# Kernel tuning notes

Measured on AMD Instinct MI355X. Metric: run time of the kernel, lower is better.

## Reference

```python
import jax, jax.numpy as jnp
import numpy as np

B, S, E = 2, 2048, 2048
H, KV, HD = 16, 4, 128  # num_heads, num_kv_heads, head_dim
G = H // KV             # query heads per kv head
ROPE_BASE = 10000.0


def rope_tables(dim, maxlen):
    freqs = 1.0 / ROPE_BASE ** (jnp.arange(0, dim, 2, dtype=jnp.float32) / dim)
    t = jnp.arange(maxlen, dtype=jnp.float32)
    f = jnp.outer(t, freqs)  # (maxlen, dim//2)
    return jnp.cos(f), jnp.sin(f)


def apply_rope(x, cos, sin):
    # x: (..., seq, heads, head_dim); interleaved-pair rotation
    s_len = x.shape[-3]
    c = cos[:s_len][:, None, :]
    s = sin[:s_len][:, None, :]
    x1 = x[..., ::2]
    x2 = x[..., 1::2]
    return jnp.stack([x1 * c - x2 * s, x1 * s + x2 * c], axis=-1).reshape(x.shape)


def setup_inputs() -> dict:
    key = jax.random.key(0)
    kx, kq, kk, kv, ko = jax.random.split(key, 5)
    x = jax.random.normal(kx, (B, S, E), dtype=jnp.float32)
    Wq = jax.random.normal(kq, (E, H * HD), dtype=jnp.float32) * 0.02
    Wk = jax.random.normal(kk, (E, KV * HD), dtype=jnp.float32) * 0.02
    Wv = jax.random.normal(kv, (E, KV * HD), dtype=jnp.float32) * 0.02
    Wo = jax.random.normal(ko, (H * HD, E), dtype=jnp.float32) * 0.02
    mask = jnp.tril(jnp.ones((S, S), dtype=bool))[None, None]  # causal (1,1,S,S)
    return {"x": x, "Wq": Wq, "Wk": Wk, "Wv": Wv, "Wo": Wo, "mask": mask}


def reference(x, Wq, Wk, Wv, Wo, mask):
    b, s, _ = x.shape
    cos, sin = rope_tables(HD, s)
    q = (x @ Wq).reshape(b, s, H, HD)
    k = (x @ Wk).reshape(b, s, KV, HD)
    v = (x @ Wv).reshape(b, s, KV, HD)
    q = apply_rope(q, cos, sin)
    k = apply_rope(k, cos, sin)
    if G > 1:
        k = jnp.repeat(k, G, axis=2)  # (b, s, H, HD)
        v = jnp.repeat(v, G, axis=2)
    q = jnp.transpose(q, (0, 2, 1, 3))  # (b, H, s, HD)
    k = jnp.transpose(k, (0, 2, 1, 3))
    v = jnp.transpose(v, (0, 2, 1, 3))
    scale = jnp.sqrt(jnp.float32(HD)).astype(q.dtype)
    scores = jnp.einsum("bhqd,bhkd->bhqk", q, k) / scale
    scores = jnp.where(mask, scores, jnp.finfo(scores.dtype).min)
    attn = jax.nn.softmax(scores, axis=-1)
    out = jnp.einsum("bhqk,bhkd->bhqd", attn, v)
    out = jnp.transpose(out, (0, 2, 1, 3)).reshape(b, s, H * HD)
    return out @ Wo
```

## Files before the change

kernel.cpp:

```cpp
#include <hip/hip_runtime.h>
#include <hip/hip_bf16.h>
#include <cstdint>

#define B_ 2
#define S_ 2048
#define E_ 2048
#define H_ 16
#define KV_ 4
#define HD_ 128
#define BS_ (B_*S_)
#define QKV_LD 3072
#define SM_SCALE 0.08838834764831845f
#define SC_LOG2E 0.1275424488538497f

typedef __attribute__((ext_vector_type(8))) __bf16 bf16x8;
typedef __attribute__((ext_vector_type(4))) float  floatx4;

__device__ __forceinline__ unsigned short f2bf(float f) {
  union { float f; unsigned u; } v; v.f = f;
  unsigned r = v.u + 0x7fffu + ((v.u >> 16) & 1u);
  return (unsigned short)(r >> 16);
}
__device__ __forceinline__ float bf2f(unsigned short u) {
  union { unsigned u; float f; } v; v.u = ((unsigned)u) << 16; return v.f;
}

__device__ __forceinline__ void async_cp16(const void* g, void* l) {
  __builtin_amdgcn_global_load_lds(
      (const __attribute__((address_space(1))) void*)g,
      (__attribute__((address_space(3))) void*)l, 16, 0, 0);
}

__global__ __launch_bounds__(256)
void cvt_bf16(const float* __restrict__ src, unsigned short* __restrict__ dst,
              int n4) {
  int idx = blockIdx.x * 256 + threadIdx.x;
  if (idx >= n4) return;
  float4 v = *(const float4*)(src + (size_t)idx * 4);
  ushort4 o;
  o.x = f2bf(v.x); o.y = f2bf(v.y); o.z = f2bf(v.z); o.w = f2bf(v.w);
  *(ushort4*)(dst + (size_t)idx * 4) = o;
}

__global__ __launch_bounds__(256)
void cvt_bf16_t(const float* __restrict__ src, unsigned short* __restrict__ dst,
                int N, int dld, int noff) {
  __shared__ float tile[64 * 65];
  const int t = threadIdx.x;
  const int bk = blockIdx.y * 64, bn = blockIdx.x * 64;
  const int r = t >> 2, cg = t & 3;
#pragma unroll
  for (int i = 0; i < 4; ++i) {
    int c = cg * 16 + i * 4;
    float4 v = *(const float4*)(src + (size_t)(bk + r) * N + bn + c);
    tile[r * 65 + c] = v.x; tile[r * 65 + c + 1] = v.y;
    tile[r * 65 + c + 2] = v.z; tile[r * 65 + c + 3] = v.w;
  }
  __syncthreads();
  const int nl = t >> 2, kg = t & 3;
  union { unsigned short u[16]; uint4 q[2]; } o;
#pragma unroll
  for (int j = 0; j < 16; ++j)
    o.u[j] = f2bf(tile[(kg * 16 + j) * 65 + nl]);
  unsigned short* dp = dst + (size_t)(noff + bn + nl) * dld + bk + kg * 16;
  *(uint4*)(dp) = o.q[0];
  *(uint4*)(dp + 8) = o.q[1];
}

__global__ __launch_bounds__(256)
void rope_kernel(unsigned short* __restrict__ qkv) {
  const int PPR = 1280;
  int idx = blockIdx.x * 256 + threadIdx.x;
  if (idx >= BS_ * PPR) return;
  int row = idx / PPR, p = idx - row * PPR;
  int col = (p < 1024) ? (2 * p) : (2048 + 2 * (p - 1024));
  int d = p & 63;
  int s = row & (S_ - 1);
  float freq = expf(-(float)d * 0.14391156831212787f);
  float ang = (float)s * freq;
  float c = cosf(ang), sn = sinf(ang);
  unsigned short* ptr = qkv + (size_t)row * QKV_LD + col;
  float x1 = bf2f(ptr[0]), x2 = bf2f(ptr[1]);
  ptr[0] = f2bf(x1 * c - x2 * sn);
  ptr[1] = f2bf(x1 * sn + x2 * c);
}

__global__ __launch_bounds__(256)
void vtrans_kernel(const unsigned short* __restrict__ qkv,
                   unsigned short* __restrict__ vt) {
  __shared__ unsigned short tile[64 * 72];
  const int tid = threadIdx.x;
  const int s0 = blockIdx.x * 64;
  const int g = blockIdx.y >> 1;
  const int hh = (blockIdx.y & 1) * 64;
  const int b = g >> 2, kvh = g & 3;
#pragma unroll
  for (int i = 0; i < 2; ++i) {
    int chunk = tid + i * 256;
    int r = chunk >> 3, c = (chunk & 7) * 8;
    uint4 v = *(const uint4*)(qkv + (size_t)(b * S_ + s0 + r) * QKV_LD + 2560 + kvh * HD_ + hh + c);
    *(uint4*)(tile + r * 72 + c) = v;
  }
  __syncthreads();
#pragma unroll
  for (int i = 0; i < 2; ++i) {
    int chunk = tid + i * 256;
    int hdr = chunk >> 3, sc = (chunk & 7) * 8;
    union { unsigned short u[8]; uint4 v; } t;
#pragma unroll
    for (int j = 0; j < 8; ++j) t.u[j] = tile[(sc + j) * 72 + hdr];
    *(uint4*)(vt + (size_t)(g * HD_ + hh + hdr) * S_ + s0 + sc) = t.v;
  }
}

template<bool OUT_BF16>
__global__ __launch_bounds__(256, 2)
void gemm_tn(const unsigned short* __restrict__ A,
             const unsigned short* __restrict__ BT,
             void* __restrict__ C, int M, int N, int K) {
  __shared__ unsigned short Ash[128 * 32];
  __shared__ unsigned short Bsh[128 * 32];
  const int tid = threadIdx.x;
  const int l = tid & 63;
  const int l16 = l & 15, l4 = l >> 4;
  const int wave = tid >> 6;
  const int wm = (wave >> 1) * 64, wn = (wave & 1) * 64;
  const int bm = blockIdx.y * 128, bn = blockIdx.x * 128;

  const int srow = l >> 2;
  const int sg = (((l & 3) - (l >> 4)) & 3) * 8;

  floatx4 acc[4][4] = {};

  for (int kb = 0; kb < K; kb += 32) {
    __syncthreads();
#pragma unroll
    for (int i = 0; i < 2; ++i) {
      int cc = wave + i * 4;
      async_cp16(A + (size_t)(bm + 16 * cc + srow) * K + kb + sg, &Ash[cc * 512]);
      async_cp16(BT + (size_t)(bn + 16 * cc + srow) * K + kb + sg, &Bsh[cc * 512]);
    }
    __syncthreads();
    bf16x8 af[4], bf[4];
#pragma unroll
    for (int t = 0; t < 4; ++t) {
      int row = wm + t * 16 + l16;
      int s = (l4 + (l16 >> 2)) & 3;
      af[t] = *(const bf16x8*)(Ash + row * 32 + s * 8);
    }
#pragma unroll
    for (int t = 0; t < 4; ++t) {
      int row = wn + t * 16 + l16;
      int s = (l4 + (l16 >> 2)) & 3;
      bf[t] = *(const bf16x8*)(Bsh + row * 32 + s * 8);
    }
#pragma unroll
    for (int tm = 0; tm < 4; ++tm)
#pragma unroll
      for (int tn = 0; tn < 4; ++tn)
        acc[tm][tn] = __builtin_amdgcn_mfma_f32_16x16x32_bf16(af[tm], bf[tn], acc[tm][tn], 0, 0, 0);
  }
#pragma unroll
  for (int tm = 0; tm < 4; ++tm)
#pragma unroll
    for (int tn = 0; tn < 4; ++tn)
#pragma unroll
      for (int r = 0; r < 4; ++r) {
        int row = bm + wm + tm * 16 + l4 * 4 + r;
        int col = bn + wn + tn * 16 + l16;
        float v = acc[tm][tn][r];
        if (OUT_BF16) ((unsigned short*)C)[(size_t)row * N + col] = f2bf(v);
        else          ((float*)C)[(size_t)row * N + col] = v;
      }
}

__global__ __launch_bounds__(256, 2)
void gqa_attention(const unsigned short* __restrict__ qkv,
                   const unsigned short* __restrict__ vt,
                   unsigned short* __restrict__ out) {
  __shared__ unsigned short Ksh[2][32 * 128];
  __shared__ unsigned short Vsh[2][128 * 32];
  __shared__ unsigned short Psh[4][16 * 40];

  const int tid = threadIdx.x, l = tid & 63, wave = tid >> 6;
  const int l16 = l & 15, l4 = l >> 4;
  const int g = blockIdx.x, b = g >> 2, kvh = g & 3;
  const int h = kvh * 4 + wave;
  const int qt = S_ - 16 - blockIdx.y * 16;
  const int nch = (qt >> 5) + 1;

  const int k_subrow = l >> 4;
  const int v_subrow = l >> 2;
  const int v_g = (((l & 3) - (l >> 4)) & 3) * 8;

  bf16x8 qf[4];
  {
    const unsigned short* qp = qkv + (size_t)(b * S_ + qt + l16) * QKV_LD + h * HD_;
#pragma unroll
    for (int c = 0; c < 4; ++c)
      qf[c] = *(const bf16x8*)(qp + c * 32 + l4 * 8);
  }
  asm volatile("s_waitcnt vmcnt(0)" ::: "memory");

#pragma unroll
  for (int i = 0; i < 2; ++i) {
    int cc = wave + i * 4;
    int gk = (((l & 15) - 4 * cc - k_subrow) & 15) * 8;
    async_cp16(qkv + (size_t)(b * S_ + 4 * cc + k_subrow) * QKV_LD + 2048 + kvh * HD_ + gk,
               &Ksh[0][cc * 512]);
    async_cp16(vt + (size_t)(g * HD_ + 16 * cc + v_subrow) * S_ + v_g,
               &Vsh[0][cc * 512]);
  }

  float m = -3e38f, lsum = 0.f;
  floatx4 acc[8] = {};

  for (int it = 0; it < nch; ++it) {
    const int kb = it * 32;
    const int cur = it & 1;
    asm volatile("s_barrier" ::: "memory");
    {
      const int kb2 = (it + 1 < nch) ? kb + 32 : 0;
#pragma unroll
      for (int i = 0; i < 2; ++i) {
        int cc = wave + i * 4;
        int gk = (((l & 15) - 4 * cc - k_subrow) & 15) * 8;
        async_cp16(qkv + (size_t)(b * S_ + kb2 + 4 * cc + k_subrow) * QKV_LD + 2048 + kvh * HD_ + gk,
                   &Ksh[cur ^ 1][cc * 512]);
        async_cp16(vt + (size_t)(g * HD_ + 16 * cc + v_subrow) * S_ + kb2 + v_g,
                   &Vsh[cur ^ 1][cc * 512]);
      }
    }
    asm volatile("s_waitcnt vmcnt(4)\n\ts_barrier" ::: "memory");

    floatx4 sacc[2] = {};
#pragma unroll
    for (int half = 0; half < 2; ++half) {
      int krow = half * 16 + l16;
#pragma unroll
      for (int c = 0; c < 4; ++c) {
        int s = (c * 4 + l4 + l16) & 15;
        bf16x8 kf = *(const bf16x8*)(&Ksh[cur][krow * 128 + s * 8]);
        sacc[half] = __builtin_amdgcn_mfma_f32_16x16x32_bf16(kf, qf[c], sacc[half], 0, 0, 0);
      }
    }
    float sv[8];
    const bool need_mask = (kb + 31 > qt);
#pragma unroll
    for (int half = 0; half < 2; ++half)
#pragma unroll
      for (int r = 0; r < 4; ++r) {
        float v = sacc[half][r] * SC_LOG2E;
        if (need_mask) {
          int ka = kb + half * 16 + l4 * 4 + r;
          if (ka > qt + l16) v = -3e38f;
        }
        sv[half * 4 + r] = v;
      }
    float mx = sv[0];
#pragma unroll
    for (int j = 1; j < 8; ++j) mx = fmaxf(mx, sv[j]);
    mx = fmaxf(mx, __shfl_xor(mx, 16, 64));
    mx = fmaxf(mx, __shfl_xor(mx, 32, 64));
    float mnew = fmaxf(m, mx);
    float p[8], psum = 0.f;
#pragma unroll
    for (int j = 0; j < 8; ++j) { p[j] = exp2f(sv[j] - mnew); psum += p[j]; }
    psum += __shfl_xor(psum, 16, 64);
    psum += __shfl_xor(psum, 32, 64);
    if (__any(mnew != m)) {
      float alpha = exp2f(m - mnew);
      lsum = lsum * alpha;
#pragma unroll
      for (int t = 0; t < 8; ++t)
#pragma unroll
        for (int r = 0; r < 4; ++r)
          acc[t][r] *= alpha;
      m = mnew;
    }
    lsum += psum;
#pragma unroll
    for (int half = 0; half < 2; ++half) {
      ushort4 pk;
      pk.x = f2bf(p[half * 4 + 0]); pk.y = f2bf(p[half * 4 + 1]);
      pk.z = f2bf(p[half * 4 + 2]); pk.w = f2bf(p[half * 4 + 3]);
      *(ushort4*)(&Psh[wave][l16 * 40 + half * 16 + l4 * 4]) = pk;
    }
    bf16x8 pf = *(const bf16x8*)(&Psh[wave][l16 * 40 + l4 * 8]);
#pragma unroll
    for (int t = 0; t < 8; ++t) {
      int row = t * 16 + l16;
      int s = (l4 + (l16 >> 2)) & 3;
      bf16x8 vf = *(const bf16x8*)(&Vsh[cur][row * 32 + s * 8]);
      acc[t] = __builtin_amdgcn_mfma_f32_16x16x32_bf16(vf, pf, acc[t], 0, 0, 0);
    }
  }

  float inv = 1.0f / lsum;
  unsigned short* op = out + (size_t)(b * S_ + qt + l16) * 2048 + h * HD_;
#pragma unroll
  for (int t = 0; t < 8; ++t) {
    ushort4 o;
    o.x = f2bf(acc[t][0] * inv); o.y = f2bf(acc[t][1] * inv);
    o.z = f2bf(acc[t][2] * inv); o.w = f2bf(acc[t][3] * inv);
    *(ushort4*)(op + t * 16 + l4 * 4) = o;
  }
}

extern "C" void kernel_launch(void* const* d_in, const int* in_sizes, int n_in,
                              void* d_out, int out_size, void* d_ws, size_t ws_size,
                              hipStream_t stream) {
  const float* x  = (const float*)d_in[0];
  const float* Wq = (const float*)d_in[1];
  const float* Wk = (const float*)d_in[2];
  const float* Wv = (const float*)d_in[3];
  const float* Wo = (const float*)d_in[4];
  float* out = (float*)d_out;

  char* ws = (char*)d_ws;
  unsigned short* xb    = (unsigned short*)(ws);
  unsigned short* wqkvT = (unsigned short*)(ws + 16777216);
  unsigned short* woT   = (unsigned short*)(ws + 29360128);
  unsigned short* qkv   = (unsigned short*)(ws + 37748736);
  unsigned short* attn  = (unsigned short*)(ws + 62914560);
  unsigned short* vt    = (unsigned short*)(ws);

  cvt_bf16<<<(4096 * 2048 / 4 + 255) / 256, 256, 0, stream>>>(x, xb, 4096 * 2048 / 4);
  cvt_bf16_t<<<dim3(32, 32), 256, 0, stream>>>(Wq, wqkvT, 2048, 2048, 0);
  cvt_bf16_t<<<dim3(8, 32),  256, 0, stream>>>(Wk, wqkvT, 512,  2048, 2048);
  cvt_bf16_t<<<dim3(8, 32),  256, 0, stream>>>(Wv, wqkvT, 512,  2048, 2560);
  cvt_bf16_t<<<dim3(32, 32), 256, 0, stream>>>(Wo, woT,  2048, 2048, 0);

  gemm_tn<true><<<dim3(24, 32), 256, 0, stream>>>(xb, wqkvT, qkv, 4096, 3072, 2048);
  rope_kernel<<<(4096 * 1280 + 255) / 256, 256, 0, stream>>>(qkv);
  vtrans_kernel<<<dim3(32, 16), 256, 0, stream>>>(qkv, vt);
  gqa_attention<<<dim3(8, 128), 256, 0, stream>>>(qkv, vt, attn);
  gemm_tn<false><<<dim3(16, 32), 256, 0, stream>>>(attn, woT, out, 4096, 2048, 2048);
}
```

Measured before the change: 353.1 us.

## Pair causal query tiles per block and widen attention blocks to eight waves

The attention kernel now runs 512 threads per block. Eight waves cover two 16-row query sub-tiles (32 rows) across the four heads of a KV group, so each loaded K/V chunk is shared by twice as many waves. Each block processes a light and a heavy causal tile in two phases (t and 63-t), which balances work across the grid, and the grid shrinks from 1024 to 256 blocks. bf16 packing now uses the paired hardware conversion intrinsic. The costs are fewer blocks in flight, larger barrier groups, and a serial two-phase loop per block.

```diff
diff --git a/kernel.cpp b/kernel.cpp
--- a/kernel.cpp
+++ b/kernel.cpp
@@ -23,6 +23,11 @@
 }
 __device__ __forceinline__ float bf2f(unsigned short u) {
   union { unsigned u; float f; } v; v.u = ((unsigned)u) << 16; return v.f;
+}
+__device__ __forceinline__ unsigned pack_bf16x2(float a, float b) {
+  union { __hip_bfloat162 h; unsigned u; } v;
+  v.h = __float22bfloat162_rn(make_float2(a, b));
+  return v.u;
 }
 
 __device__ __forceinline__ void async_cp16(const void* g, void* l) {
@@ -174,136 +179,133 @@
       }
 }
 
-__global__ __launch_bounds__(256, 2)
+__global__ __launch_bounds__(512, 2)
 void gqa_attention(const unsigned short* __restrict__ qkv,
                    const unsigned short* __restrict__ vt,
                    unsigned short* __restrict__ out) {
   __shared__ unsigned short Ksh[2][32 * 128];
   __shared__ unsigned short Vsh[2][128 * 32];
-  __shared__ unsigned short Psh[4][16 * 40];
+  __shared__ unsigned short Psh[8][16 * 40];
 
   const int tid = threadIdx.x, l = tid & 63, wave = tid >> 6;
   const int l16 = l & 15, l4 = l >> 4;
   const int g = blockIdx.x, b = g >> 2, kvh = g & 3;
-  const int h = kvh * 4 + wave;
-  const int qt = S_ - 16 - blockIdx.y * 16;
-  const int nch = (qt >> 5) + 1;
-
-  const int k_subrow = l >> 4;
-  const int v_subrow = l >> 2;
-  const int v_g = (((l & 3) - (l >> 4)) & 3) * 8;
-
-  bf16x8 qf[4];
-  {
-    const unsigned short* qp = qkv + (size_t)(b * S_ + qt + l16) * QKV_LD + h * HD_;
-#pragma unroll
-    for (int c = 0; c < 4; ++c)
-      qf[c] = *(const bf16x8*)(qp + c * 32 + l4 * 8);
-  }
-  asm volatile("s_waitcnt vmcnt(0)" ::: "memory");
-
-#pragma unroll
-  for (int i = 0; i < 2; ++i) {
-    int cc = wave + i * 4;
-    int gk = (((l & 15) - 4 * cc - k_subrow) & 15) * 8;
-    async_cp16(qkv + (size_t)(b * S_ + 4 * cc + k_subrow) * QKV_LD + 2048 + kvh * HD_ + gk,
-               &Ksh[0][cc * 512]);
-    async_cp16(vt + (size_t)(g * HD_ + 16 * cc + v_subrow) * S_ + v_g,
-               &Vsh[0][cc * 512]);
-  }
-
-  float m = -3e38f, lsum = 0.f;
-  floatx4 acc[8] = {};
-
-  for (int it = 0; it < nch; ++it) {
-    const int kb = it * 32;
-    const int cur = it & 1;
+  const int wh = wave & 3, wq = wave >> 2;
+  const int h = kvh * 4 + wh;
+
+  const int k_row = 4 * wave + (l >> 4);
+  const int gk = (((l & 15) - k_row) & 15) * 8;
+  const int v_row = 16 * wave + (l >> 2);
+  const int gv = (((l & 3) - (l >> 4)) & 3) * 8;
+
+  for (int phase = 0; phase < 2; ++phase) {
+    const int t = phase ? (63 - (int)blockIdx.y) : (int)blockIdx.y;
+    const int qt = t * 32 + wq * 16;
+    const int nch = t + 1;
+
+    bf16x8 qf[4];
+    {
+      const unsigned short* qp = qkv + (size_t)(b * S_ + qt + l16) * QKV_LD + h * HD_;
+#pragma unroll
+      for (int c = 0; c < 4; ++c)
+        qf[c] = *(const bf16x8*)(qp + c * 32 + l4 * 8);
+    }
+    asm volatile("s_waitcnt vmcnt(0)" ::: "memory");
+
+    async_cp16(qkv + (size_t)(b * S_ + k_row) * QKV_LD + 2048 + kvh * HD_ + gk,
+               &Ksh[0][wave * 512]);
+    async_cp16(vt + (size_t)(g * HD_ + v_row) * S_ + gv,
+               &Vsh[0][wave * 512]);
+
+    float m = -3e38f, lsum = 0.f;
+    floatx4 acc[8] = {};
+
+    for (int it = 0; it < nch; ++it) {
+      const int kb = it * 32;
+      const int cur = it & 1;
+      asm volatile("s_barrier" ::: "memory");
+      {
+        const int kb2 = (it + 1 < nch) ? kb + 32 : 0;
+        async_cp16(qkv + (size_t)(b * S_ + kb2 + k_row) * QKV_LD + 2048 + kvh * HD_ + gk,
+                   &Ksh[cur ^ 1][wave * 512]);
+        async_cp16(vt + (size_t)(g * HD_ + v_row) * S_ + kb2 + gv,
+                   &Vsh[cur ^ 1][wave * 512]);
+      }
+      asm volatile("s_waitcnt vmcnt(2)\n\ts_barrier" ::: "memory");
+
+      floatx4 sacc[2] = {};
+#pragma unroll
+      for (int half = 0; half < 2; ++half) {
+        int krow = half * 16 + l16;
+#pragma unroll
+        for (int c = 0; c < 4; ++c) {
+          int s = (c * 4 + l4 + l16) & 15;
+          bf16x8 kf = *(const bf16x8*)(&Ksh[cur][krow * 128 + s * 8]);
+          sacc[half] = __builtin_amdgcn_mfma_f32_16x16x32_bf16(kf, qf[c], sacc[half], 0, 0, 0);
+        }
+      }
+      float sv[8];
+      const bool need_mask = (kb + 31 > qt);
+#pragma unroll
+      for (int half = 0; half < 2; ++half)
+#pragma unroll
+        for (int r = 0; r < 4; ++r) {
+          float v = sacc[half][r] * SC_LOG2E;
+          if (need_mask) {
+            int ka = kb + half * 16 + l4 * 4 + r;
+            if (ka > qt + l16) v = -3e38f;
+          }
+          sv[half * 4 + r] = v;
+        }
+      float mx = sv[0];
+#pragma unroll
+      for (int j = 1; j < 8; ++j) mx = fmaxf(mx, sv[j]);
+      mx = fmaxf(mx, __shfl_xor(mx, 16, 64));
+      mx = fmaxf(mx, __shfl_xor(mx, 32, 64));
+      float mnew = fmaxf(m, mx);
+      float p[8], psum = 0.f;
+#pragma unroll
+      for (int j = 0; j < 8; ++j) { p[j] = exp2f(sv[j] - mnew); psum += p[j]; }
+      psum += __shfl_xor(psum, 16, 64);
+      psum += __shfl_xor(psum, 32, 64);
+      if (__any(mnew != m)) {
+        float alpha = exp2f(m - mnew);
+        lsum = lsum * alpha;
+#pragma unroll
+        for (int u = 0; u < 8; ++u)
+#pragma unroll
+          for (int r = 0; r < 4; ++r)
+            acc[u][r] *= alpha;
+        m = mnew;
+      }
+      lsum += psum;
+#pragma unroll
+      for (int half = 0; half < 2; ++half) {
+        uint2 pk;
+        pk.x = pack_bf16x2(p[half * 4 + 0], p[half * 4 + 1]);
+        pk.y = pack_bf16x2(p[half * 4 + 2], p[half * 4 + 3]);
+        *(uint2*)(&Psh[wave][l16 * 40 + half * 16 + l4 * 4]) = pk;
+      }
+      bf16x8 pf = *(const bf16x8*)(&Psh[wave][l16 * 40 + l4 * 8]);
+#pragma unroll
+      for (int u = 0; u < 8; ++u) {
+        int row = u * 16 + l16;
+        int s = (l4 + (l16 >> 2)) & 3;
+        bf16x8 vf = *(const bf16x8*)(&Vsh[cur][row * 32 + s * 8]);
+        acc[u] = __builtin_amdgcn_mfma_f32_16x16x32_bf16(vf, pf, acc[u], 0, 0, 0);
+      }
+    }
     asm volatile("s_barrier" ::: "memory");
-    {
-      const int kb2 = (it + 1 < nch) ? kb + 32 : 0;
-#pragma unroll
-      for (int i = 0; i < 2; ++i) {
-        int cc = wave + i * 4;
-        int gk = (((l & 15) - 4 * cc - k_subrow) & 15) * 8;
-        async_cp16(qkv + (size_t)(b * S_ + kb2 + 4 * cc + k_subrow) * QKV_LD + 2048 + kvh * HD_ + gk,
-                   &Ksh[cur ^ 1][cc * 512]);
-        async_cp16(vt + (size_t)(g * HD_ + 16 * cc + v_subrow) * S_ + kb2 + v_g,
-                   &Vsh[cur ^ 1][cc * 512]);
-      }
-    }
-    asm volatile("s_waitcnt vmcnt(4)\n\ts_barrier" ::: "memory");
-
-    floatx4 sacc[2] = {};
-#pragma unroll
-    for (int half = 0; half < 2; ++half) {
-      int krow = half * 16 + l16;
-#pragma unroll
-      for (int c = 0; c < 4; ++c) {
-        int s = (c * 4 + l4 + l16) & 15;
-        bf16x8 kf = *(const bf16x8*)(&Ksh[cur][krow * 128 + s * 8]);
-        sacc[half] = __builtin_amdgcn_mfma_f32_16x16x32_bf16(kf, qf[c], sacc[half], 0, 0, 0);
-      }
-    }
-    float sv[8];
-    const bool need_mask = (kb + 31 > qt);
-#pragma unroll
-    for (int half = 0; half < 2; ++half)
-#pragma unroll
-      for (int r = 0; r < 4; ++r) {
-        float v = sacc[half][r] * SC_LOG2E;
-        if (need_mask) {
-          int ka = kb + half * 16 + l4 * 4 + r;
-          if (ka > qt + l16) v = -3e38f;
-        }
-        sv[half * 4 + r] = v;
-      }
-    float mx = sv[0];
-#pragma unroll
-    for (int j = 1; j < 8; ++j) mx = fmaxf(mx, sv[j]);
-    mx = fmaxf(mx, __shfl_xor(mx, 16, 64));
-    mx = fmaxf(mx, __shfl_xor(mx, 32, 64));
-    float mnew = fmaxf(m, mx);
-    float p[8], psum = 0.f;
-#pragma unroll
-    for (int j = 0; j < 8; ++j) { p[j] = exp2f(sv[j] - mnew); psum += p[j]; }
-    psum += __shfl_xor(psum, 16, 64);
-    psum += __shfl_xor(psum, 32, 64);
-    if (__any(mnew != m)) {
-      float alpha = exp2f(m - mnew);
-      lsum = lsum * alpha;
-#pragma unroll
-      for (int t = 0; t < 8; ++t)
-#pragma unroll
-        for (int r = 0; r < 4; ++r)
-          acc[t][r] *= alpha;
-      m = mnew;
-    }
-    lsum += psum;
-#pragma unroll
-    for (int half = 0; half < 2; ++half) {
-      ushort4 pk;
-      pk.x = f2bf(p[half * 4 + 0]); pk.y = f2bf(p[half * 4 + 1]);
-      pk.z = f2bf(p[half * 4 + 2]); pk.w = f2bf(p[half * 4 + 3]);
-      *(ushort4*)(&Psh[wave][l16 * 40 + half * 16 + l4 * 4]) = pk;
-    }
-    bf16x8 pf = *(const bf16x8*)(&Psh[wave][l16 * 40 + l4 * 8]);
-#pragma unroll
-    for (int t = 0; t < 8; ++t) {
-      int row = t * 16 + l16;
-      int s = (l4 + (l16 >> 2)) & 3;
-      bf16x8 vf = *(const bf16x8*)(&Vsh[cur][row * 32 + s * 8]);
-      acc[t] = __builtin_amdgcn_mfma_f32_16x16x32_bf16(vf, pf, acc[t], 0, 0, 0);
-    }
-  }
-
-  float inv = 1.0f / lsum;
-  unsigned short* op = out + (size_t)(b * S_ + qt + l16) * 2048 + h * HD_;
-#pragma unroll
-  for (int t = 0; t < 8; ++t) {
-    ushort4 o;
-    o.x = f2bf(acc[t][0] * inv); o.y = f2bf(acc[t][1] * inv);
-    o.z = f2bf(acc[t][2] * inv); o.w = f2bf(acc[t][3] * inv);
-    *(ushort4*)(op + t * 16 + l4 * 4) = o;
+
+    float inv = 1.0f / lsum;
+    unsigned short* op = out + (size_t)(b * S_ + qt + l16) * 2048 + h * HD_;
+#pragma unroll
+    for (int u = 0; u < 8; ++u) {
+      uint2 o;
+      o.x = pack_bf16x2(acc[u][0] * inv, acc[u][1] * inv);
+      o.y = pack_bf16x2(acc[u][2] * inv, acc[u][3] * inv);
+      *(uint2*)(op + u * 16 + l4 * 4) = o;
+    }
   }
 }
 
@@ -334,6 +336,6 @@
   gemm_tn<true><<<dim3(24, 32), 256, 0, stream>>>(xb, wqkvT, qkv, 4096, 3072, 2048);
   rope_kernel<<<(4096 * 1280 + 255) / 256, 256, 0, stream>>>(qkv);
   vtrans_kernel<<<dim3(32, 16), 256, 0, stream>>>(qkv, vt);
-  gqa_attention<<<dim3(8, 128), 256, 0, stream>>>(qkv, vt, attn);
+  gqa_attention<<<dim3(8, 32), 512, 0, stream>>>(qkv, vt, attn);
   gemm_tn<false><<<dim3(16, 32), 256, 0, stream>>>(attn, woT, out, 4096, 2048, 2048);
 }
```

Result: slower. 361.3 us (+2.3%).
